# Performance work log

Hardware: AMD Instinct MI355X
Metric: run time of the kernel (lower is better)

## Reference

```python
import jax, jax.numpy as jnp
import numpy as np

B, N, C = 4, 2048, 128
H = 4
HD = C // H
SCALE = HD ** -0.5
NEG = -9e15


def setup_inputs() -> dict:
    key = jax.random.key(0)
    ks = jax.random.split(key, 6)
    x = jax.random.normal(ks[0], (B, N, C), dtype=jnp.float32)
    A = jax.random.randint(ks[1], (N, N), 0, 2, dtype=jnp.int32)
    std = 0.02
    Wq = jax.random.normal(ks[2], (C, C), dtype=jnp.float32) * std
    Wkv = jax.random.normal(ks[3], (2 * C, C), dtype=jnp.float32) * std
    Wp = jax.random.normal(ks[4], (C, C), dtype=jnp.float32) * std
    bp = jnp.zeros((C,), dtype=jnp.float32)
    return {"x": x, "A": A, "Wq": Wq, "Wkv": Wkv, "Wp": Wp, "bp": bp}


def reference(x, A, Wq, Wkv, Wp, bp):
    # q/k/v projections (torch Linear: x @ W.T)
    q = (x @ Wq.T).reshape(B, N, H, HD).transpose(0, 2, 1, 3)      # [B,H,N,HD]
    kv = (x @ Wkv.T).reshape(B, N, 2, H, HD).transpose(2, 0, 3, 1, 4)
    k, v = kv[0], kv[1]                                            # [B,H,N,HD]
    attn = jnp.einsum('bhnd,bhmd->bhnm', q, k) * SCALE             # [B,H,N,N]
    attn = jnp.where(A > 0, attn, NEG)                             # adjacency mask
    attn = jax.nn.softmax(attn, axis=-1)
    out = jnp.einsum('bhnm,bhmd->bhnd', attn, v)                   # [B,H,N,HD]
    out = out.transpose(0, 2, 1, 3).reshape(B, N, C)
    out = out @ Wp.T + bp
    return out + x                                                 # residual
```

## Files before the change

kernel.cpp:

```cpp
#include <hip/hip_runtime.h>
#include <math.h>

constexpr int kB = 4, kN = 2048, kC = 128, kH = 4, kHD = 32;
constexpr float kScaleLog2e = 0.17677669529663687f * 1.4426950408889634f;

typedef __attribute__((ext_vector_type(8))) short bf16x8;
typedef __attribute__((ext_vector_type(4))) float f32x4;

__device__ __forceinline__ float exp2fast(float x) { return __builtin_amdgcn_exp2f(x); }
__device__ __forceinline__ unsigned int cvtpk(float lo, float hi) {
  unsigned int r;
  asm("v_cvt_pk_bf16_f32 %0, %1, %2" : "=v"(r) : "v"(lo), "v"(hi));
  return r;
}
__device__ __forceinline__ float bflo(unsigned int u) {
  union { unsigned int u; float f; } v; v.u = u << 16; return v.f;
}
__device__ __forceinline__ float bfhi(unsigned int u) {
  union { unsigned int u; float f; } v; v.u = u & 0xFFFF0000u; return v.f;
}

__global__ __launch_bounds__(256) void qkv_abit_kernel(
    const float* __restrict__ x, const float* __restrict__ Wq,
    const float* __restrict__ Wkv, const int* __restrict__ A,
    unsigned short* __restrict__ qws, unsigned short* __restrict__ kws,
    unsigned short* __restrict__ vtws, unsigned long long* __restrict__ Abits) {
  const int bid = blockIdx.x;
  const int t = threadIdx.x;
  if (bid >= 512) {
    const int lane = t & 63;
    const int w0 = (bid - 512) * 4 + (t >> 6);
    for (int idx = w0; idx < kN * 32; idx += 2048) {
      const int row = idx >> 5, c0 = (idx & 31) * 64;
      unsigned long long msk = __ballot(A[(size_t)row * kN + c0 + lane] > 0);
      if (lane == 0) Abits[idx] = msk;
    }
    return;
  }
  __shared__ unsigned short xs[16][136];
  const int row0 = bid * 16;
  const int b = row0 >> 11;
  {
    const int r = t >> 4, c = (t & 15) * 8;
    const float* src = x + (size_t)(row0 + r) * kC + c;
    float4 a = *(const float4*)src;
    float4 bb = *(const float4*)(src + 4);
    *(uint4*)&xs[r][c] = make_uint4(cvtpk(a.x, a.y), cvtpk(a.z, a.w),
                                    cvtpk(bb.x, bb.y), cvtpk(bb.z, bb.w));
  }
  __syncthreads();
  const int w = t >> 6, l = t & 63, lr = l & 15, g = l >> 4;
  bf16x8 xf[4];
  #pragma unroll
  for (int s = 0; s < 4; ++s) xf[s] = *(const bf16x8*)&xs[lr][s * 32 + g * 8];
  #pragma unroll
  for (int ci = 0; ci < 6; ++ci) {
    const int c0 = (w * 6 + ci) * 16;
    const float* wrow = (c0 < 128) ? (Wq + (size_t)(c0 + lr) * kC)
                                   : (Wkv + (size_t)(c0 - 128 + lr) * kC);
    f32x4 acc = {0.f, 0.f, 0.f, 0.f};
    if (c0 < 256) {
      #pragma unroll
      for (int s = 0; s < 4; ++s) {
        const float* wp = wrow + s * 32 + g * 8;
        float4 wa = *(const float4*)wp, wb = *(const float4*)(wp + 4);
        union { uint4 u; bf16x8 v; } cw;
        cw.u = make_uint4(cvtpk(wa.x, wa.y), cvtpk(wa.z, wa.w),
                          cvtpk(wb.x, wb.y), cvtpk(wb.z, wb.w));
        acc = __builtin_amdgcn_mfma_f32_16x16x32_bf16(cw.v, xf[s], acc, 0, 0, 0);
      }
      if (c0 < 128) {
        #pragma unroll
        for (int i = 0; i < 4; ++i) acc[i] *= kScaleLog2e;
      }
      const int col0 = c0 + g * 4;
      const int h = (col0 & 127) >> 5, hd0 = col0 & 31;
      unsigned short* dst = (col0 < 128) ? qws : kws;
      uint2 pk = make_uint2(cvtpk(acc[0], acc[1]), cvtpk(acc[2], acc[3]));
      *(uint2*)&dst[((size_t)(b * kH + h) * kN + row0 + lr) * kHD + hd0] = pk;
    } else {
      #pragma unroll
      for (int s = 0; s < 4; ++s) {
        const float* wp = wrow + s * 32 + g * 8;
        float4 wa = *(const float4*)wp, wb = *(const float4*)(wp + 4);
        union { uint4 u; bf16x8 v; } cw;
        cw.u = make_uint4(cvtpk(wa.x, wa.y), cvtpk(wa.z, wa.w),
                          cvtpk(wb.x, wb.y), cvtpk(wb.z, wb.w));
        acc = __builtin_amdgcn_mfma_f32_16x16x32_bf16(xf[s], cw.v, acc, 0, 0, 0);
      }
      const int d = (c0 - 256) + lr;
      uint2 pk = make_uint2(cvtpk(acc[0], acc[1]), cvtpk(acc[2], acc[3]));
      *(uint2*)&vtws[((size_t)(b * kH + (d >> 5)) * kHD + (d & 31)) * kN + row0 + g * 4] = pk;
    }
  }
}

__global__ __launch_bounds__(256) void attn_kernel(
    const unsigned short* __restrict__ qws, const unsigned short* __restrict__ kws,
    const unsigned short* __restrict__ vtws,
    const unsigned long long* __restrict__ Abits,
    unsigned short* __restrict__ Opart, float* __restrict__ lws, int tiles) {
  __shared__ unsigned short Ksf[2][4][64][8];
  __shared__ unsigned short Vtf[2][2][2][64][8];
  __shared__ unsigned short Psf[4][2][2][64][8];
  const int t = threadIdx.x, w = t >> 6, l = t & 63, lr = l & 15, g = l >> 4;
  const int bh = blockIdx.y, q0 = blockIdx.x * 128, z = blockIdx.z;
  const int qa = q0 + w * 32 + lr, qb = qa + 16;
  const int kt0 = z * tiles;
  const unsigned short* kbase = kws + (size_t)bh * kN * kHD;
  const unsigned short* vbase = vtws + (size_t)bh * kHD * kN;
  bf16x8 qf0 = *(const bf16x8*)&qws[((size_t)bh * kN + qa) * kHD + g * 8];
  bf16x8 qf1 = *(const bf16x8*)&qws[((size_t)bh * kN + qb) * kHD + g * 8];
  const unsigned long long* arow0 = Abits + (size_t)qa * (kN / 64);
  const unsigned long long* arow1 = Abits + (size_t)qb * (kN / 64);

  const int skc = t >> 6, sl = t & 63;
  const size_t koff = ((size_t)(skc * 16 + (sl & 15))) * kHD + (sl >> 4) * 8;
  const int sdh = t >> 7, sct = (t >> 6) & 1;
  const size_t voff = ((size_t)(sdh * 16 + (sl & 15))) * kN + sct * 32 + (sl >> 4) * 8;

  bf16x8 kreg = *(const bf16x8*)(kbase + (size_t)kt0 * 64 * kHD + koff);
  bf16x8 vreg = *(const bf16x8*)(vbase + (size_t)kt0 * 64 + voff);
  *(bf16x8*)&Ksf[0][skc][sl][0] = kreg;
  *(bf16x8*)&Vtf[0][sdh][sct][sl][0] = vreg;
  unsigned long long mw0 = arow0[kt0], mw1 = arow1[kt0], mw0n = 0, mw1n = 0;

  f32x4 o0a = {0.f, 0.f, 0.f, 0.f}, o1a = o0a, o2a = o0a;
  f32x4 o0b = o0a, o1b = o0a, o2b = o0a;
  bf16x8 ones;
  #pragma unroll
  for (int i = 0; i < 8; ++i) ones[i] = (short)0x3F80;
  const int gsh = g * 4;
  unsigned short* const psw0 = &Psf[w][0][0][0][0];
  unsigned short* const psw1 = &Psf[w][1][0][0][0];
  const int pbase = (((g >> 1) << 4) | lr) * 8 + (g & 1) * 4;

  for (int it = 0; it < tiles; ++it) {
    const int c = it & 1;
    const int kt = kt0 + it;
    __syncthreads();
    if (it + 1 < tiles) {
      kreg = *(const bf16x8*)(kbase + (size_t)(kt + 1) * 64 * kHD + koff);
      vreg = *(const bf16x8*)(vbase + (size_t)(kt + 1) * 64 + voff);
      mw0n = arow0[kt + 1];
      mw1n = arow1[kt + 1];
    }
    const unsigned int wlo0 = ((unsigned int)mw0) >> gsh;
    const unsigned int whi0 = ((unsigned int)(mw0 >> 32)) >> gsh;
    const unsigned int wlo1 = ((unsigned int)mw1) >> gsh;
    const unsigned int whi1 = ((unsigned int)(mw1 >> 32)) >> gsh;

    #pragma unroll
    for (int kc = 0; kc < 4; ++kc) {
      bf16x8 kf = *(const bf16x8*)&Ksf[c][kc][l][0];
      f32x4 z4 = {0.f, 0.f, 0.f, 0.f};
      f32x4 acc0 = __builtin_amdgcn_mfma_f32_16x16x32_bf16(kf, qf0, z4, 0, 0, 0);
      f32x4 acc1 = __builtin_amdgcn_mfma_f32_16x16x32_bf16(kf, qf1, z4, 0, 0, 0);
      const unsigned int word0 = (kc < 2) ? wlo0 : whi0;
      const unsigned int word1 = (kc < 2) ? wlo1 : whi1;
      float p0[4], p1[4];
      #pragma unroll
      for (int i = 0; i < 4; ++i) {
        float e0 = exp2fast(acc0[i]);
        float e1 = exp2fast(acc1[i]);
        int m0, m1;
        asm("v_bfe_i32 %0, %1, %2, 1" : "=v"(m0) : "v"(word0), "n"((kc & 1) * 16 + i));
        asm("v_bfe_i32 %0, %1, %2, 1" : "=v"(m1) : "v"(word1), "n"((kc & 1) * 16 + i));
        union { float f; int u; } u0, u1;
        u0.f = e0; u0.u &= m0; p0[i] = u0.f;
        u1.f = e1; u1.u &= m1; p1[i] = u1.f;
      }
      *(uint2*)(psw0 + kc * 256 + pbase) =
          make_uint2(cvtpk(p0[0], p0[1]), cvtpk(p0[2], p0[3]));
      *(uint2*)(psw1 + kc * 256 + pbase) =
          make_uint2(cvtpk(p1[0], p1[1]), cvtpk(p1[2], p1[3]));
    }
    #pragma unroll
    for (int ct = 0; ct < 2; ++ct) {
      bf16x8 pf0 = *(const bf16x8*)&Psf[w][0][ct][l][0];
      bf16x8 pf1 = *(const bf16x8*)&Psf[w][1][ct][l][0];
      bf16x8 va = *(const bf16x8*)&Vtf[c][0][ct][l][0];
      bf16x8 vb = *(const bf16x8*)&Vtf[c][1][ct][l][0];
      o0a = __builtin_amdgcn_mfma_f32_16x16x32_bf16(va, pf0, o0a, 0, 0, 0);
      o1a = __builtin_amdgcn_mfma_f32_16x16x32_bf16(vb, pf0, o1a, 0, 0, 0);
      o2a = __builtin_amdgcn_mfma_f32_16x16x32_bf16(ones, pf0, o2a, 0, 0, 0);
      o0b = __builtin_amdgcn_mfma_f32_16x16x32_bf16(va, pf1, o0b, 0, 0, 0);
      o1b = __builtin_amdgcn_mfma_f32_16x16x32_bf16(vb, pf1, o1b, 0, 0, 0);
      o2b = __builtin_amdgcn_mfma_f32_16x16x32_bf16(ones, pf1, o2b, 0, 0, 0);
    }
    if (it + 1 < tiles) {
      *(bf16x8*)&Ksf[c ^ 1][skc][sl][0] = kreg;
      *(bf16x8*)&Vtf[c ^ 1][sdh][sct][sl][0] = vreg;
      mw0 = mw0n;
      mw1 = mw1n;
    }
  }

  unsigned short* orow0 = Opart + ((size_t)(z * 16 + bh) * kN + qa) * kHD;
  unsigned short* orow1 = Opart + ((size_t)(z * 16 + bh) * kN + qb) * kHD;
  *(uint2*)&orow0[g * 4]      = make_uint2(cvtpk(o0a[0], o0a[1]), cvtpk(o0a[2], o0a[3]));
  *(uint2*)&orow0[16 + g * 4] = make_uint2(cvtpk(o1a[0], o1a[1]), cvtpk(o1a[2], o1a[3]));
  *(uint2*)&orow1[g * 4]      = make_uint2(cvtpk(o0b[0], o0b[1]), cvtpk(o0b[2], o0b[3]));
  *(uint2*)&orow1[16 + g * 4] = make_uint2(cvtpk(o1b[0], o1b[1]), cvtpk(o1b[2], o1b[3]));
  if (g == 0) {
    lws[(size_t)(z * 16 + bh) * kN + qa] = o2a[0];
    lws[(size_t)(z * 16 + bh) * kN + qb] = o2b[0];
  }
}

__global__ __launch_bounds__(256) void proj_kernel(
    const unsigned short* __restrict__ Opart, const float* __restrict__ lws,
    const float* __restrict__ Wp, const float* __restrict__ bp,
    const float* __restrict__ x, float* __restrict__ out, int np) {
  const int t = threadIdx.x, w = t >> 6, l = t & 63, lr = l & 15, g = l >> 4;
  const int row0 = blockIdx.x * 16;
  const int b = row0 >> 11;
  bf16x8 af[4];
  #pragma unroll
  for (int s = 0; s < 4; ++s) {
    const int bh = b * kH + s;
    float a0 = 0.f, a1 = 0.f, a2 = 0.f, a3 = 0.f, a4 = 0.f, a5 = 0.f, a6 = 0.f, a7 = 0.f;
    float lacc = 0.f;
    for (int p = 0; p < np; ++p) {
      const size_t base = (size_t)(p * 16 + bh) * kN + row0 + lr;
      const uint4 u = *(const uint4*)&Opart[base * kHD + g * 8];
      lacc += lws[base];
      a0 += bflo(u.x); a1 += bfhi(u.x);
      a2 += bflo(u.y); a3 += bfhi(u.y);
      a4 += bflo(u.z); a5 += bfhi(u.z);
      a6 += bflo(u.w); a7 += bfhi(u.w);
    }
    const float inv = 1.f / fmaxf(lacc, 1e-30f);
    union { uint4 u; bf16x8 v; } cv;
    cv.u = make_uint4(cvtpk(a0 * inv, a1 * inv), cvtpk(a2 * inv, a3 * inv),
                      cvtpk(a4 * inv, a5 * inv), cvtpk(a6 * inv, a7 * inv));
    af[s] = cv.v;
  }
  #pragma unroll
  for (int ci = 0; ci < 2; ++ci) {
    const int c0 = (w * 2 + ci) * 16;
    const float* wrow = Wp + (size_t)(c0 + lr) * kC;
    f32x4 acc = {0.f, 0.f, 0.f, 0.f};
    #pragma unroll
    for (int s = 0; s < 4; ++s) {
      const float* wp = wrow + s * 32 + g * 8;
      float4 wa = *(const float4*)wp, wb = *(const float4*)(wp + 4);
      union { uint4 u; bf16x8 v; } cw;
      cw.u = make_uint4(cvtpk(wa.x, wa.y), cvtpk(wa.z, wa.w),
                        cvtpk(wb.x, wb.y), cvtpk(wb.z, wb.w));
      acc = __builtin_amdgcn_mfma_f32_16x16x32_bf16(cw.v, af[s], acc, 0, 0, 0);
    }
    const int col0 = c0 + g * 4;
    const size_t off = (size_t)(row0 + lr) * kC + col0;
    const float4 xb = *(const float4*)&x[off];
    const float4 bb = *(const float4*)&bp[col0];
    float4 r;
    r.x = acc[0] + bb.x + xb.x;
    r.y = acc[1] + bb.y + xb.y;
    r.z = acc[2] + bb.z + xb.z;
    r.w = acc[3] + bb.w + xb.w;
    *(float4*)&out[off] = r;
  }
}

extern "C" void kernel_launch(void* const* d_in, const int* in_sizes, int n_in,
                              void* d_out, int out_size, void* d_ws, size_t ws_size,
                              hipStream_t stream) {
  const float* x   = (const float*)d_in[0];
  const int*   A   = (const int*)d_in[1];
  const float* Wq  = (const float*)d_in[2];
  const float* Wkv = (const float*)d_in[3];
  const float* Wp  = (const float*)d_in[4];
  const float* bp  = (const float*)d_in[5];
  float* out = (float*)d_out;
  char* ws = (char*)d_ws;

  unsigned short* qws   = (unsigned short*)(ws);
  unsigned short* kws   = (unsigned short*)(ws + (2u << 20));
  unsigned short* vtws  = (unsigned short*)(ws + (4u << 20));
  unsigned long long* Abits = (unsigned long long*)(ws + (6u << 20));
  float*          lws   = (float*)(ws + (7u << 20));
  unsigned short* Opart = (unsigned short*)(ws + (8u << 20));

  const int np = (ws_size >= (16u << 20)) ? 4 : 1;
  const int tiles = 32 / np;

  qkv_abit_kernel<<<dim3(1024), dim3(256), 0, stream>>>(
      x, Wq, Wkv, A, qws, kws, vtws, Abits);
  attn_kernel<<<dim3(16, 16, np), dim3(256), 0, stream>>>(
      qws, kws, vtws, Abits, Opart, lws, tiles);
  proj_kernel<<<dim3(512), dim3(256), 0, stream>>>(Opart, lws, Wp, bp, x, out, np);
}
```

Baseline: 63.06 us.

## Preconvert weights to bf16, drop LDS staging of K/V in attention

```diff
diff --git a/kernel.cpp b/kernel.cpp
--- a/kernel.cpp
+++ b/kernel.cpp
@@ -7,7 +7,7 @@
 typedef __attribute__((ext_vector_type(8))) short bf16x8;
 typedef __attribute__((ext_vector_type(4))) float f32x4;
 
-__device__ __forceinline__ float exp2fast(float x) { return __builtin_amdgcn_exp2f(x); }
+__device__ __forceinline__ float exp2fast(float v) { return __builtin_amdgcn_exp2f(v); }
 __device__ __forceinline__ unsigned int cvtpk(float lo, float hi) {
   unsigned int r;
   asm("v_cvt_pk_bf16_f32 %0, %1, %2" : "=v"(r) : "v"(lo), "v"(hi));
@@ -20,25 +20,48 @@
   union { unsigned int u; float f; } v; v.u = u & 0xFFFF0000u; return v.f;
 }
 
-__global__ __launch_bounds__(256) void qkv_abit_kernel(
-    const float* __restrict__ x, const float* __restrict__ Wq,
-    const float* __restrict__ Wkv, const int* __restrict__ A,
-    unsigned short* __restrict__ qws, unsigned short* __restrict__ kws,
-    unsigned short* __restrict__ vtws, unsigned long long* __restrict__ Abits) {
+__global__ __launch_bounds__(256) void prep_kernel(
+    const int* __restrict__ A, const float* __restrict__ Wq,
+    const float* __restrict__ Wkv, const float* __restrict__ Wp,
+    unsigned long long* __restrict__ Abits, unsigned short* __restrict__ Wallb,
+    unsigned short* __restrict__ Wpb) {
   const int bid = blockIdx.x;
-  const int t = threadIdx.x;
-  if (bid >= 512) {
-    const int lane = t & 63;
-    const int w0 = (bid - 512) * 4 + (t >> 6);
-    for (int idx = w0; idx < kN * 32; idx += 2048) {
+  if (bid < 512) {
+    const int lane = threadIdx.x & 63;
+    const int w0 = bid * 4 + (threadIdx.x >> 6);
+    #pragma unroll 4
+    for (int k = 0; k < 32; ++k) {
+      const int idx = w0 + k * 2048;
       const int row = idx >> 5, c0 = (idx & 31) * 64;
       unsigned long long msk = __ballot(A[(size_t)row * kN + c0 + lane] > 0);
       if (lane == 0) Abits[idx] = msk;
     }
-    return;
-  }
+  } else {
+    const int i4 = ((bid - 512) * 256 + threadIdx.x) * 4;
+    float4 v;
+    unsigned short* dst;
+    if (i4 < 16384) {
+      v = *(const float4*)&Wq[i4];
+      v.x *= kScaleLog2e; v.y *= kScaleLog2e; v.z *= kScaleLog2e; v.w *= kScaleLog2e;
+      dst = Wallb + i4;
+    } else if (i4 < 49152) {
+      v = *(const float4*)&Wkv[i4 - 16384];
+      dst = Wallb + i4;
+    } else {
+      v = *(const float4*)&Wp[i4 - 49152];
+      dst = Wpb + (i4 - 49152);
+    }
+    *(uint2*)dst = make_uint2(cvtpk(v.x, v.y), cvtpk(v.z, v.w));
+  }
+}
+
+__global__ __launch_bounds__(256) void qkv_kernel(
+    const float* __restrict__ x, const unsigned short* __restrict__ Wallb,
+    unsigned short* __restrict__ qws, unsigned short* __restrict__ kws,
+    unsigned short* __restrict__ vtws) {
   __shared__ unsigned short xs[16][136];
-  const int row0 = bid * 16;
+  const int t = threadIdx.x;
+  const int row0 = blockIdx.x * 16;
   const int b = row0 >> 11;
   {
     const int r = t >> 4, c = (t & 15) * 8;
@@ -56,22 +79,13 @@
   #pragma unroll
   for (int ci = 0; ci < 6; ++ci) {
     const int c0 = (w * 6 + ci) * 16;
-    const float* wrow = (c0 < 128) ? (Wq + (size_t)(c0 + lr) * kC)
-                                   : (Wkv + (size_t)(c0 - 128 + lr) * kC);
+    const unsigned short* wr = Wallb + (size_t)(c0 + lr) * kC + g * 8;
     f32x4 acc = {0.f, 0.f, 0.f, 0.f};
     if (c0 < 256) {
       #pragma unroll
       for (int s = 0; s < 4; ++s) {
-        const float* wp = wrow + s * 32 + g * 8;
-        float4 wa = *(const float4*)wp, wb = *(const float4*)(wp + 4);
-        union { uint4 u; bf16x8 v; } cw;
-        cw.u = make_uint4(cvtpk(wa.x, wa.y), cvtpk(wa.z, wa.w),
-                          cvtpk(wb.x, wb.y), cvtpk(wb.z, wb.w));
-        acc = __builtin_amdgcn_mfma_f32_16x16x32_bf16(cw.v, xf[s], acc, 0, 0, 0);
-      }
-      if (c0 < 128) {
-        #pragma unroll
-        for (int i = 0; i < 4; ++i) acc[i] *= kScaleLog2e;
+        bf16x8 wf = *(const bf16x8*)(wr + s * 32);
+        acc = __builtin_amdgcn_mfma_f32_16x16x32_bf16(wf, xf[s], acc, 0, 0, 0);
       }
       const int col0 = c0 + g * 4;
       const int h = (col0 & 127) >> 5, hd0 = col0 & 31;
@@ -81,12 +95,8 @@
     } else {
       #pragma unroll
       for (int s = 0; s < 4; ++s) {
-        const float* wp = wrow + s * 32 + g * 8;
-        float4 wa = *(const float4*)wp, wb = *(const float4*)(wp + 4);
-        union { uint4 u; bf16x8 v; } cw;
-        cw.u = make_uint4(cvtpk(wa.x, wa.y), cvtpk(wa.z, wa.w),
-                          cvtpk(wb.x, wb.y), cvtpk(wb.z, wb.w));
-        acc = __builtin_amdgcn_mfma_f32_16x16x32_bf16(xf[s], cw.v, acc, 0, 0, 0);
+        bf16x8 wf = *(const bf16x8*)(wr + s * 32);
+        acc = __builtin_amdgcn_mfma_f32_16x16x32_bf16(xf[s], wf, acc, 0, 0, 0);
       }
       const int d = (c0 - 256) + lr;
       uint2 pk = make_uint2(cvtpk(acc[0], acc[1]), cvtpk(acc[2], acc[3]));
@@ -95,35 +105,26 @@
   }
 }
 
-__global__ __launch_bounds__(256) void attn_kernel(
+__global__ __launch_bounds__(256, 4) void attn_kernel(
     const unsigned short* __restrict__ qws, const unsigned short* __restrict__ kws,
     const unsigned short* __restrict__ vtws,
     const unsigned long long* __restrict__ Abits,
     unsigned short* __restrict__ Opart, float* __restrict__ lws, int tiles) {
-  __shared__ unsigned short Ksf[2][4][64][8];
-  __shared__ unsigned short Vtf[2][2][2][64][8];
   __shared__ unsigned short Psf[4][2][2][64][8];
   const int t = threadIdx.x, w = t >> 6, l = t & 63, lr = l & 15, g = l >> 4;
-  const int bh = blockIdx.y, q0 = blockIdx.x * 128, z = blockIdx.z;
+  const int bh = blockIdx.x, qblk = blockIdx.y, z = blockIdx.z;
+  const int q0 = qblk * 128;
   const int qa = q0 + w * 32 + lr, qb = qa + 16;
   const int kt0 = z * tiles;
-  const unsigned short* kbase = kws + (size_t)bh * kN * kHD;
-  const unsigned short* vbase = vtws + (size_t)bh * kHD * kN;
+  const unsigned short* kfp = kws + (size_t)bh * kN * kHD +
+                              ((size_t)kt0 * 64 + lr) * kHD + g * 8;
+  const unsigned short* vfp0 = vtws + (size_t)bh * kHD * kN + (size_t)lr * kN +
+                               kt0 * 64 + g * 8;
+  const unsigned short* vfp1 = vfp0 + (size_t)16 * kN;
   bf16x8 qf0 = *(const bf16x8*)&qws[((size_t)bh * kN + qa) * kHD + g * 8];
   bf16x8 qf1 = *(const bf16x8*)&qws[((size_t)bh * kN + qb) * kHD + g * 8];
-  const unsigned long long* arow0 = Abits + (size_t)qa * (kN / 64);
-  const unsigned long long* arow1 = Abits + (size_t)qb * (kN / 64);
-
-  const int skc = t >> 6, sl = t & 63;
-  const size_t koff = ((size_t)(skc * 16 + (sl & 15))) * kHD + (sl >> 4) * 8;
-  const int sdh = t >> 7, sct = (t >> 6) & 1;
-  const size_t voff = ((size_t)(sdh * 16 + (sl & 15))) * kN + sct * 32 + (sl >> 4) * 8;
-
-  bf16x8 kreg = *(const bf16x8*)(kbase + (size_t)kt0 * 64 * kHD + koff);
-  bf16x8 vreg = *(const bf16x8*)(vbase + (size_t)kt0 * 64 + voff);
-  *(bf16x8*)&Ksf[0][skc][sl][0] = kreg;
-  *(bf16x8*)&Vtf[0][sdh][sct][sl][0] = vreg;
-  unsigned long long mw0 = arow0[kt0], mw1 = arow1[kt0], mw0n = 0, mw1n = 0;
+  const unsigned long long* arow0 = Abits + (size_t)qa * (kN / 64) + kt0;
+  const unsigned long long* arow1 = Abits + (size_t)qb * (kN / 64) + kt0;
 
   f32x4 o0a = {0.f, 0.f, 0.f, 0.f}, o1a = o0a, o2a = o0a;
   f32x4 o0b = o0a, o1b = o0a, o2b = o0a;
@@ -135,24 +136,19 @@
   unsigned short* const psw1 = &Psf[w][1][0][0][0];
   const int pbase = (((g >> 1) << 4) | lr) * 8 + (g & 1) * 4;
 
+  #pragma unroll 2
   for (int it = 0; it < tiles; ++it) {
-    const int c = it & 1;
-    const int kt = kt0 + it;
-    __syncthreads();
-    if (it + 1 < tiles) {
-      kreg = *(const bf16x8*)(kbase + (size_t)(kt + 1) * 64 * kHD + koff);
-      vreg = *(const bf16x8*)(vbase + (size_t)(kt + 1) * 64 + voff);
-      mw0n = arow0[kt + 1];
-      mw1n = arow1[kt + 1];
-    }
+    const unsigned long long mw0 = arow0[it];
+    const unsigned long long mw1 = arow1[it];
     const unsigned int wlo0 = ((unsigned int)mw0) >> gsh;
     const unsigned int whi0 = ((unsigned int)(mw0 >> 32)) >> gsh;
     const unsigned int wlo1 = ((unsigned int)mw1) >> gsh;
     const unsigned int whi1 = ((unsigned int)(mw1 >> 32)) >> gsh;
+    const unsigned short* ktb = kfp + (size_t)it * 64 * kHD;
 
     #pragma unroll
     for (int kc = 0; kc < 4; ++kc) {
-      bf16x8 kf = *(const bf16x8*)&Ksf[c][kc][l][0];
+      bf16x8 kf = *(const bf16x8*)(ktb + (size_t)(kc * 16) * kHD);
       f32x4 z4 = {0.f, 0.f, 0.f, 0.f};
       f32x4 acc0 = __builtin_amdgcn_mfma_f32_16x16x32_bf16(kf, qf0, z4, 0, 0, 0);
       f32x4 acc1 = __builtin_amdgcn_mfma_f32_16x16x32_bf16(kf, qf1, z4, 0, 0, 0);
@@ -175,24 +171,20 @@
       *(uint2*)(psw1 + kc * 256 + pbase) =
           make_uint2(cvtpk(p1[0], p1[1]), cvtpk(p1[2], p1[3]));
     }
+    const unsigned short* vtb0 = vfp0 + it * 64;
+    const unsigned short* vtb1 = vfp1 + it * 64;
     #pragma unroll
     for (int ct = 0; ct < 2; ++ct) {
       bf16x8 pf0 = *(const bf16x8*)&Psf[w][0][ct][l][0];
       bf16x8 pf1 = *(const bf16x8*)&Psf[w][1][ct][l][0];
-      bf16x8 va = *(const bf16x8*)&Vtf[c][0][ct][l][0];
-      bf16x8 vb = *(const bf16x8*)&Vtf[c][1][ct][l][0];
+      bf16x8 va = *(const bf16x8*)(vtb0 + ct * 32);
+      bf16x8 vb = *(const bf16x8*)(vtb1 + ct * 32);
       o0a = __builtin_amdgcn_mfma_f32_16x16x32_bf16(va, pf0, o0a, 0, 0, 0);
       o1a = __builtin_amdgcn_mfma_f32_16x16x32_bf16(vb, pf0, o1a, 0, 0, 0);
       o2a = __builtin_amdgcn_mfma_f32_16x16x32_bf16(ones, pf0, o2a, 0, 0, 0);
       o0b = __builtin_amdgcn_mfma_f32_16x16x32_bf16(va, pf1, o0b, 0, 0, 0);
       o1b = __builtin_amdgcn_mfma_f32_16x16x32_bf16(vb, pf1, o1b, 0, 0, 0);
       o2b = __builtin_amdgcn_mfma_f32_16x16x32_bf16(ones, pf1, o2b, 0, 0, 0);
-    }
-    if (it + 1 < tiles) {
-      *(bf16x8*)&Ksf[c ^ 1][skc][sl][0] = kreg;
-      *(bf16x8*)&Vtf[c ^ 1][sdh][sct][sl][0] = vreg;
-      mw0 = mw0n;
-      mw1 = mw1n;
     }
   }
 
@@ -210,7 +202,7 @@
 
 __global__ __launch_bounds__(256) void proj_kernel(
     const unsigned short* __restrict__ Opart, const float* __restrict__ lws,
-    const float* __restrict__ Wp, const float* __restrict__ bp,
+    const unsigned short* __restrict__ Wpb, const float* __restrict__ bp,
     const float* __restrict__ x, float* __restrict__ out, int np) {
   const int t = threadIdx.x, w = t >> 6, l = t & 63, lr = l & 15, g = l >> 4;
   const int row0 = blockIdx.x * 16;
@@ -239,16 +231,12 @@
   #pragma unroll
   for (int ci = 0; ci < 2; ++ci) {
     const int c0 = (w * 2 + ci) * 16;
-    const float* wrow = Wp + (size_t)(c0 + lr) * kC;
+    const unsigned short* wr = Wpb + (size_t)(c0 + lr) * kC + g * 8;
     f32x4 acc = {0.f, 0.f, 0.f, 0.f};
     #pragma unroll
     for (int s = 0; s < 4; ++s) {
-      const float* wp = wrow + s * 32 + g * 8;
-      float4 wa = *(const float4*)wp, wb = *(const float4*)(wp + 4);
-      union { uint4 u; bf16x8 v; } cw;
-      cw.u = make_uint4(cvtpk(wa.x, wa.y), cvtpk(wa.z, wa.w),
-                        cvtpk(wb.x, wb.y), cvtpk(wb.z, wb.w));
-      acc = __builtin_amdgcn_mfma_f32_16x16x32_bf16(cw.v, af[s], acc, 0, 0, 0);
+      bf16x8 wf = *(const bf16x8*)(wr + s * 32);
+      acc = __builtin_amdgcn_mfma_f32_16x16x32_bf16(wf, af[s], acc, 0, 0, 0);
     }
     const int col0 = c0 + g * 4;
     const size_t off = (size_t)(row0 + lr) * kC + col0;
@@ -279,15 +267,17 @@
   unsigned short* kws   = (unsigned short*)(ws + (2u << 20));
   unsigned short* vtws  = (unsigned short*)(ws + (4u << 20));
   unsigned long long* Abits = (unsigned long long*)(ws + (6u << 20));
+  unsigned short* Wallb = (unsigned short*)(ws + (6u << 20) + (1u << 19));
+  unsigned short* Wpb   = Wallb + 384 * 128;
   float*          lws   = (float*)(ws + (7u << 20));
   unsigned short* Opart = (unsigned short*)(ws + (8u << 20));
 
   const int np = (ws_size >= (16u << 20)) ? 4 : 1;
   const int tiles = 32 / np;
 
-  qkv_abit_kernel<<<dim3(1024), dim3(256), 0, stream>>>(
-      x, Wq, Wkv, A, qws, kws, vtws, Abits);
+  prep_kernel<<<dim3(576), dim3(256), 0, stream>>>(A, Wq, Wkv, Wp, Abits, Wallb, Wpb);
+  qkv_kernel<<<dim3(512), dim3(256), 0, stream>>>(x, Wallb, qws, kws, vtws);
   attn_kernel<<<dim3(16, 16, np), dim3(256), 0, stream>>>(
       qws, kws, vtws, Abits, Opart, lws, tiles);
-  proj_kernel<<<dim3(512), dim3(256), 0, stream>>>(Opart, lws, Wp, bp, x, out, np);
-}
+  proj_kernel<<<dim3(512), dim3(256), 0, stream>>>(Opart, lws, Wpb, bp, x, out, np);
+}
```

After: 67.53 us. +7.1%, slower.

## Load K/V fragments directly from global, drop LDS staging and block syncs

Applied to the files above, without the earlier changes.

```diff
diff --git a/kernel.cpp b/kernel.cpp
--- a/kernel.cpp
+++ b/kernel.cpp
@@ -7,7 +7,7 @@
 typedef __attribute__((ext_vector_type(8))) short bf16x8;
 typedef __attribute__((ext_vector_type(4))) float f32x4;
 
-__device__ __forceinline__ float exp2fast(float x) { return __builtin_amdgcn_exp2f(x); }
+__device__ __forceinline__ float exp2fast(float v) { return __builtin_amdgcn_exp2f(v); }
 __device__ __forceinline__ unsigned int cvtpk(float lo, float hi) {
   unsigned int r;
   asm("v_cvt_pk_bf16_f32 %0, %1, %2" : "=v"(r) : "v"(lo), "v"(hi));
@@ -30,7 +30,9 @@
   if (bid >= 512) {
     const int lane = t & 63;
     const int w0 = (bid - 512) * 4 + (t >> 6);
-    for (int idx = w0; idx < kN * 32; idx += 2048) {
+    #pragma unroll 4
+    for (int k = 0; k < 32; ++k) {
+      const int idx = w0 + k * 2048;
       const int row = idx >> 5, c0 = (idx & 31) * 64;
       unsigned long long msk = __ballot(A[(size_t)row * kN + c0 + lane] > 0);
       if (lane == 0) Abits[idx] = msk;
@@ -95,38 +97,30 @@
   }
 }
 
-__global__ __launch_bounds__(256) void attn_kernel(
+__global__ __launch_bounds__(256, 4) void attn_kernel(
     const unsigned short* __restrict__ qws, const unsigned short* __restrict__ kws,
     const unsigned short* __restrict__ vtws,
     const unsigned long long* __restrict__ Abits,
     unsigned short* __restrict__ Opart, float* __restrict__ lws, int tiles) {
-  __shared__ unsigned short Ksf[2][4][64][8];
-  __shared__ unsigned short Vtf[2][2][2][64][8];
   __shared__ unsigned short Psf[4][2][2][64][8];
   const int t = threadIdx.x, w = t >> 6, l = t & 63, lr = l & 15, g = l >> 4;
-  const int bh = blockIdx.y, q0 = blockIdx.x * 128, z = blockIdx.z;
+  const int bh = blockIdx.x, qblk = blockIdx.y, z = blockIdx.z;
+  const int q0 = qblk * 128;
   const int qa = q0 + w * 32 + lr, qb = qa + 16;
   const int kt0 = z * tiles;
-  const unsigned short* kbase = kws + (size_t)bh * kN * kHD;
-  const unsigned short* vbase = vtws + (size_t)bh * kHD * kN;
+  const unsigned short* kfp = kws + (size_t)bh * kN * kHD +
+                              ((size_t)kt0 * 64 + lr) * kHD + g * 8;
+  const unsigned short* vfp0 = vtws + (size_t)bh * kHD * kN + (size_t)lr * kN +
+                               kt0 * 64 + g * 8;
+  const unsigned short* vfp1 = vfp0 + (size_t)16 * kN;
   bf16x8 qf0 = *(const bf16x8*)&qws[((size_t)bh * kN + qa) * kHD + g * 8];
   bf16x8 qf1 = *(const bf16x8*)&qws[((size_t)bh * kN + qb) * kHD + g * 8];
-  const unsigned long long* arow0 = Abits + (size_t)qa * (kN / 64);
-  const unsigned long long* arow1 = Abits + (size_t)qb * (kN / 64);
-
-  const int skc = t >> 6, sl = t & 63;
-  const size_t koff = ((size_t)(skc * 16 + (sl & 15))) * kHD + (sl >> 4) * 8;
-  const int sdh = t >> 7, sct = (t >> 6) & 1;
-  const size_t voff = ((size_t)(sdh * 16 + (sl & 15))) * kN + sct * 32 + (sl >> 4) * 8;
-
-  bf16x8 kreg = *(const bf16x8*)(kbase + (size_t)kt0 * 64 * kHD + koff);
-  bf16x8 vreg = *(const bf16x8*)(vbase + (size_t)kt0 * 64 + voff);
-  *(bf16x8*)&Ksf[0][skc][sl][0] = kreg;
-  *(bf16x8*)&Vtf[0][sdh][sct][sl][0] = vreg;
-  unsigned long long mw0 = arow0[kt0], mw1 = arow1[kt0], mw0n = 0, mw1n = 0;
+  const unsigned long long* arow0 = Abits + (size_t)qa * (kN / 64) + kt0;
+  const unsigned long long* arow1 = Abits + (size_t)qb * (kN / 64) + kt0;
 
   f32x4 o0a = {0.f, 0.f, 0.f, 0.f}, o1a = o0a, o2a = o0a;
   f32x4 o0b = o0a, o1b = o0a, o2b = o0a;
+  const f32x4 kZero = {0.f, 0.f, 0.f, 0.f};
   bf16x8 ones;
   #pragma unroll
   for (int i = 0; i < 8; ++i) ones[i] = (short)0x3F80;
@@ -135,27 +129,21 @@
   unsigned short* const psw1 = &Psf[w][1][0][0][0];
   const int pbase = (((g >> 1) << 4) | lr) * 8 + (g & 1) * 4;
 
+  #pragma unroll 2
   for (int it = 0; it < tiles; ++it) {
-    const int c = it & 1;
-    const int kt = kt0 + it;
-    __syncthreads();
-    if (it + 1 < tiles) {
-      kreg = *(const bf16x8*)(kbase + (size_t)(kt + 1) * 64 * kHD + koff);
-      vreg = *(const bf16x8*)(vbase + (size_t)(kt + 1) * 64 + voff);
-      mw0n = arow0[kt + 1];
-      mw1n = arow1[kt + 1];
-    }
+    const unsigned long long mw0 = arow0[it];
+    const unsigned long long mw1 = arow1[it];
     const unsigned int wlo0 = ((unsigned int)mw0) >> gsh;
     const unsigned int whi0 = ((unsigned int)(mw0 >> 32)) >> gsh;
     const unsigned int wlo1 = ((unsigned int)mw1) >> gsh;
     const unsigned int whi1 = ((unsigned int)(mw1 >> 32)) >> gsh;
+    const unsigned short* ktb = kfp + (size_t)it * 64 * kHD;
 
     #pragma unroll
     for (int kc = 0; kc < 4; ++kc) {
-      bf16x8 kf = *(const bf16x8*)&Ksf[c][kc][l][0];
-      f32x4 z4 = {0.f, 0.f, 0.f, 0.f};
-      f32x4 acc0 = __builtin_amdgcn_mfma_f32_16x16x32_bf16(kf, qf0, z4, 0, 0, 0);
-      f32x4 acc1 = __builtin_amdgcn_mfma_f32_16x16x32_bf16(kf, qf1, z4, 0, 0, 0);
+      bf16x8 kf = *(const bf16x8*)(ktb + (size_t)(kc * 16) * kHD);
+      f32x4 acc0 = __builtin_amdgcn_mfma_f32_16x16x32_bf16(kf, qf0, kZero, 0, 0, 0);
+      f32x4 acc1 = __builtin_amdgcn_mfma_f32_16x16x32_bf16(kf, qf1, kZero, 0, 0, 0);
       const unsigned int word0 = (kc < 2) ? wlo0 : whi0;
       const unsigned int word1 = (kc < 2) ? wlo1 : whi1;
       float p0[4], p1[4];
@@ -175,12 +163,15 @@
       *(uint2*)(psw1 + kc * 256 + pbase) =
           make_uint2(cvtpk(p1[0], p1[1]), cvtpk(p1[2], p1[3]));
     }
+    const unsigned short* vtb0 = vfp0 + it * 64;
+    const unsigned short* vtb1 = vfp1 + it * 64;
+    __builtin_amdgcn_s_setprio(1);
     #pragma unroll
     for (int ct = 0; ct < 2; ++ct) {
       bf16x8 pf0 = *(const bf16x8*)&Psf[w][0][ct][l][0];
       bf16x8 pf1 = *(const bf16x8*)&Psf[w][1][ct][l][0];
-      bf16x8 va = *(const bf16x8*)&Vtf[c][0][ct][l][0];
-      bf16x8 vb = *(const bf16x8*)&Vtf[c][1][ct][l][0];
+      bf16x8 va = *(const bf16x8*)(vtb0 + ct * 32);
+      bf16x8 vb = *(const bf16x8*)(vtb1 + ct * 32);
       o0a = __builtin_amdgcn_mfma_f32_16x16x32_bf16(va, pf0, o0a, 0, 0, 0);
       o1a = __builtin_amdgcn_mfma_f32_16x16x32_bf16(vb, pf0, o1a, 0, 0, 0);
       o2a = __builtin_amdgcn_mfma_f32_16x16x32_bf16(ones, pf0, o2a, 0, 0, 0);
@@ -188,12 +179,7 @@
       o1b = __builtin_amdgcn_mfma_f32_16x16x32_bf16(vb, pf1, o1b, 0, 0, 0);
       o2b = __builtin_amdgcn_mfma_f32_16x16x32_bf16(ones, pf1, o2b, 0, 0, 0);
     }
-    if (it + 1 < tiles) {
-      *(bf16x8*)&Ksf[c ^ 1][skc][sl][0] = kreg;
-      *(bf16x8*)&Vtf[c ^ 1][sdh][sct][sl][0] = vreg;
-      mw0 = mw0n;
-      mw1 = mw1n;
-    }
+    __builtin_amdgcn_s_setprio(0);
   }
 
   unsigned short* orow0 = Opart + ((size_t)(z * 16 + bh) * kN + qa) * kHD;
@@ -279,10 +265,10 @@
   unsigned short* kws   = (unsigned short*)(ws + (2u << 20));
   unsigned short* vtws  = (unsigned short*)(ws + (4u << 20));
   unsigned long long* Abits = (unsigned long long*)(ws + (6u << 20));
-  float*          lws   = (float*)(ws + (7u << 20));
-  unsigned short* Opart = (unsigned short*)(ws + (8u << 20));
-
-  const int np = (ws_size >= (16u << 20)) ? 4 : 1;
+  float*          lws   = (float*)(ws + (6u << 20) + (1u << 19));
+  unsigned short* Opart = (unsigned short*)(ws + (16u << 20));
+
+  const int np = (ws_size >= (32u << 20)) ? 8 : 1;
   const int tiles = 32 / np;
 
   qkv_abit_kernel<<<dim3(1024), dim3(256), 0, stream>>>(
```

Result: slower. 77.40 us (+22.7%).
